# Kernel optimization log

Measured on AMD Instinct MI355X. Metric: run time of the kernel, lower is better.

## Reference

```python
import jax, jax.numpy as jnp
import numpy as np

THRESHOLD = 0.35
NEGPOS_RATIO = 7
VAR0, VAR1 = 0.1, 0.2
NUM_CLASSES = 2


def point_form(pr):
    # center-size [cx,cy,w,h] -> corner [x1,y1,x2,y2]
    return jnp.concatenate([pr[:, :2] - pr[:, 2:] / 2, pr[:, :2] + pr[:, 2:] / 2], axis=1)


def jaccard(a, b):
    # a: [A,4] corner boxes, b: [P,4] corner boxes -> IoU [A,P]
    lt = jnp.maximum(a[:, None, :2], b[None, :, :2])
    rb = jnp.minimum(a[:, None, 2:], b[None, :, 2:])
    wh = jnp.clip(rb - lt, 0.0)
    inter = wh[..., 0] * wh[..., 1]
    area_a = ((a[:, 2] - a[:, 0]) * (a[:, 3] - a[:, 1]))[:, None]
    area_b = ((b[:, 2] - b[:, 0]) * (b[:, 3] - b[:, 1]))[None, :]
    return inter / (area_a + area_b - inter)


def match_one(truths, landms, labels, priors_pf, priors):
    # truths [A,4] corner, landms [A,10], labels [A], priors [P,4] center-size
    A = truths.shape[0]
    overlaps = jaccard(truths, priors_pf)                       # [A,P]
    best_prior_idx = jnp.argmax(overlaps, axis=1)               # [A]
    best_truth_overlap = jnp.max(overlaps, axis=0)              # [P]
    best_truth_idx = jnp.argmax(overlaps, axis=0)               # [P]
    # ensure every gt matches its best prior
    best_truth_overlap = best_truth_overlap.at[best_prior_idx].set(2.0)
    best_truth_idx = best_truth_idx.at[best_prior_idx].set(jnp.arange(A))
    matches = truths[best_truth_idx]                            # [P,4]
    conf = labels[best_truth_idx].astype(jnp.int32)             # [P]
    conf = jnp.where(best_truth_overlap < THRESHOLD, 0, conf)
    # encode loc targets
    g_cxcy = ((matches[:, :2] + matches[:, 2:]) / 2 - priors[:, :2]) / (VAR0 * priors[:, 2:])
    g_wh = jnp.log((matches[:, 2:] - matches[:, :2]) / priors[:, 2:]) / VAR1
    loc = jnp.concatenate([g_cxcy, g_wh], axis=1)               # [P,4]
    # encode landmark targets (5 points)
    ml = landms[best_truth_idx].reshape(-1, 5, 2)               # [P,5,2]
    g_lm = (ml - priors[:, None, :2]) / (VAR0 * priors[:, None, 2:])
    landm = g_lm.reshape(-1, 10)                                # [P,10]
    return loc, conf, landm


def setup_inputs() -> dict:
    key = jax.random.key(0)
    kL, kC, kF, kp1, kp2, kc, ks, klm = jax.random.split(key, 8)
    B, P, A = 32, 131072, 32
    loc_data = jax.random.normal(kL, (B, P, 4), dtype=jnp.float32)
    conf_data = jax.random.normal(kC, (B, P, NUM_CLASSES), dtype=jnp.float32)
    loc_five_data = jax.random.normal(kF, (B, P, 10), dtype=jnp.float32)
    # priors in center-size form with positive w,h
    p_cxy = jax.random.uniform(kp1, (P, 2), minval=0.0, maxval=1.0)
    p_wh = jax.random.uniform(kp2, (P, 2), minval=0.02, maxval=0.3)
    priors = jnp.concatenate([p_cxy, p_wh], axis=1).astype(jnp.float32)
    # targets: [B, A, 15] = 4 corner box coords, 1 label (=1), 10 landmark coords
    g_cxy = jax.random.uniform(kc, (B, A, 2), minval=0.1, maxval=0.9)
    g_wh = jax.random.uniform(ks, (B, A, 2), minval=0.05, maxval=0.4)
    boxes = jnp.concatenate([g_cxy - g_wh / 2, g_cxy + g_wh / 2], axis=-1)
    lbl = jnp.ones((B, A, 1), dtype=jnp.float32)
    lms = jax.random.uniform(klm, (B, A, 10), minval=0.0, maxval=1.0)
    targets = jnp.concatenate([boxes, lbl, lms], axis=-1).astype(jnp.float32)
    return {"loc_data": loc_data, "conf_data": conf_data,
            "loc_five_data": loc_five_data, "priors": priors, "targets": targets}


def multibox_loss(loc_data, conf_data, loc_five_data, priors, targets):
    B, P = loc_data.shape[0], priors.shape[0]
    truths = targets[..., :4]      # [B,A,4]
    labels = targets[..., 4]       # [B,A]
    landms = targets[..., 5:]      # [B,A,10]
    priors_pf = point_form(priors)
    loc_t, conf_t, landm_t = jax.vmap(match_one, in_axes=(0, 0, 0, None, None))(
        truths, landms, labels, priors_pf, priors)   # [B,P,4], [B,P], [B,P,10]

    pos = conf_t > 0               # [B,P]
    posf = pos.astype(loc_data.dtype)

    # localization: smooth L1, sum over positives
    d = loc_data - loc_t
    sl1 = jnp.where(jnp.abs(d) < 1.0, 0.5 * d * d, jnp.abs(d) - 0.5)
    loss_l = jnp.sum(sl1 * posf[..., None])

    # landmarks: MSE, sum over positives
    d5 = loc_five_data - landm_t
    loss_coords = jnp.sum(d5 * d5 * posf[..., None])

    # per-prior classification loss for hard negative mining
    lse = jax.nn.logsumexp(conf_data, axis=-1)                                  # [B,P]
    gt_logit = jnp.take_along_axis(conf_data, conf_t[..., None], axis=-1)[..., 0]
    loss_c_all = lse - gt_logit                                                 # [B,P]
    loss_mine = jnp.where(pos, 0.0, loss_c_all)
    # double-argsort rank trick
    loss_idx = jnp.argsort(-loss_mine, axis=1)
    idx_rank = jnp.argsort(loss_idx, axis=1)
    num_pos = jnp.sum(pos.astype(jnp.int32), axis=1, keepdims=True)             # [B,1]
    num_neg = jnp.minimum(NEGPOS_RATIO * num_pos, P - 1)
    neg = idx_rank < num_neg

    sel = (pos | neg).astype(conf_data.dtype)
    loss_c = jnp.sum(loss_c_all * sel)

    N = jnp.maximum(jnp.sum(num_pos).astype(loc_data.dtype), 1.0)
    return loss_l / N, loss_c / N, loss_coords / N


def reference(loc_data, conf_data, loc_five_data, priors, targets):
    return multibox_loss(loc_data, conf_data, loc_five_data, priors, targets)
```

## Files before the change

### kernel.cpp

```cpp
#include <hip/hip_runtime.h>
#include <stdint.h>
#include <math.h>

#define PP 131072
#define BB 32
#define AA 32
#define THRESH 0.35f

static constexpr size_t OFF_ACCL = 0;
static constexpr size_t OFF_ACCC = 256;
static constexpr size_t OFF_ACCLM = 512;
static constexpr size_t OFF_NP = 768;
static constexpr size_t OFF_SLOT = 1024;
static constexpr size_t OFF_SEL = 9216;
static constexpr size_t OFF_BTI = 16384;
static constexpr size_t OFF_HIST = OFF_BTI;
static constexpr size_t OFF_LM = 16384 + (size_t)BB * PP;

__global__ __launch_bounds__(256) void k_match(
    const float* __restrict__ priors, const float* __restrict__ targets,
    unsigned long long* __restrict__ slots, unsigned char* __restrict__ bti) {
#pragma clang fp contract(off)
  const int b = blockIdx.y;
  const int tid = threadIdx.x;
  __shared__ float tx0[AA], ty0[AA], tx1[AA], ty1[AA], tar[AA];
  if (tid < AA) {
    const float* tg = targets + ((size_t)b * AA + tid) * 15;
    float a0 = tg[0], a1 = tg[1], a2 = tg[2], a3 = tg[3];
    tx0[tid] = a0; ty0[tid] = a1; tx1[tid] = a2; ty1[tid] = a3;
    tar[tid] = (a2 - a0) * (a3 - a1);
  }
  __syncthreads();

  const int base = blockIdx.x * 2048;
  float px0[8], py0[8], px1[8], py1[8], areaB[8];
  float cbi[8], cbd[8];
  int cba[8];
#pragma unroll
  for (int i = 0; i < 8; ++i) {
    const int p = base + i * 256 + tid;
    const float4 pr = reinterpret_cast<const float4*>(priors)[p];
    const float hx = pr.z * 0.5f, hy = pr.w * 0.5f;
    px0[i] = pr.x - hx; py0[i] = pr.y - hy;
    px1[i] = pr.x + hx; py1[i] = pr.y + hy;
    areaB[i] = (px1[i] - px0[i]) * (py1[i] - py0[i]);
    cbi[i] = -1.f; cbd[i] = 1.f; cba[i] = 0;
  }

  const int lane = tid & 63;
  for (int a = 0; a < AA; ++a) {
    const float sx0 = tx0[a], sy0 = ty0[a], sx1 = tx1[a], sy1 = ty1[a];
    const float sar = tar[a];
    float bi = -1.f, bd = 1.f;
    int bp = 0;
#pragma unroll
    for (int i = 0; i < 8; ++i) {
      const float lx = fmaxf(sx0, px0[i]);
      const float ly = fmaxf(sy0, py0[i]);
      const float rx = fminf(sx1, px1[i]);
      const float ry = fminf(sy1, py1[i]);
      const float wx = fmaxf(rx - lx, 0.f);
      const float wy = fmaxf(ry - ly, 0.f);
      const float inter = wx * wy;
      const float den = sar + areaB[i] - inter;
      if (inter * cbd[i] > cbi[i] * den) { cbi[i] = inter; cbd[i] = den; cba[i] = a; }
      if (inter * bd > bi * den) { bi = inter; bd = den; bp = base + i * 256 + tid; }
    }
    const float r = bi / bd;
    unsigned long long key =
        ((unsigned long long)__float_as_uint(r) << 32) |
        (unsigned long long)(0xFFFFFFFFu - (unsigned)bp);
#pragma unroll
    for (int off = 1; off < 64; off <<= 1) {
      unsigned long long o = __shfl_xor(key, off, 64);
      if (o > key) key = o;
    }
    if (lane == 0) atomicMax(&slots[b * AA + a], key);
  }

#pragma unroll
  for (int i = 0; i < 8; ++i) {
    const int p = base + i * 256 + tid;
    const float r = cbi[i] / cbd[i];
    bti[(size_t)b * PP + p] =
        (unsigned char)cba[i] | ((r < THRESH) ? 0 : 32);
  }
}

__global__ __launch_bounds__(256) void k_loss(
    const float* __restrict__ loc, const float* __restrict__ conf,
    const float* __restrict__ loc5, const float* __restrict__ priors,
    const float* __restrict__ targets,
    const unsigned long long* __restrict__ slots,
    const unsigned char* __restrict__ bti, float* __restrict__ lossm,
    double* __restrict__ accL, double* __restrict__ accC,
    double* __restrict__ accLM, int* __restrict__ numpos) {
#pragma clang fp contract(off)
  const int b = blockIdx.y;
  const int tid = threadIdx.x;
  __shared__ float tr[AA][15];
  __shared__ int ovr[AA];
  if (tid < AA) {
    const float* tg = targets + ((size_t)b * AA + tid) * 15;
#pragma unroll
    for (int j = 0; j < 15; ++j) tr[tid][j] = tg[j];
    const unsigned long long key = slots[b * AA + tid];
    ovr[tid] = (int)(0xFFFFFFFFu - (unsigned)(key & 0xFFFFFFFFull));
  }
  __syncthreads();
  int ov[AA];
#pragma unroll
  for (int a = 0; a < AA; ++a) ov[a] = ovr[a];

  double ll = 0.0, lc = 0.0, lm = 0.0;
  int np = 0;
  const int base = blockIdx.x * 2048;
  for (int it = 0; it < 8; ++it) {
    const int p = base + it * 256 + tid;
    const size_t gp = (size_t)b * PP + p;
    const unsigned char f = bti[gp];
    int idx = f & 31;
    bool posf = (f & 32) != 0;
#pragma unroll
    for (int a = 0; a < AA; ++a)
      if (ov[a] == p) { idx = a; posf = true; }
    const int cls = posf ? (int)tr[idx][4] : 0;
    const bool pos = cls > 0;

    const float2 cc = reinterpret_cast<const float2*>(conf)[gp];
    const float mx = fmaxf(cc.x, cc.y);
    const float lse = mx + logf(expf(cc.x - mx) + expf(cc.y - mx));
    const float gtl = (cls >= 1) ? cc.y : cc.x;
    const float lca = lse - gtl;
    lossm[gp] = pos ? 0.f : lca;

    if (pos) {
      ++np;
      lc += (double)lca;
      const float4 pr = reinterpret_cast<const float4*>(priors)[p];
      const float m0 = tr[idx][0], m1 = tr[idx][1];
      const float m2 = tr[idx][2], m3 = tr[idx][3];
      const float vx = 0.1f * pr.z, vy = 0.1f * pr.w;
      const float t0 = ((m0 + m2) / 2.0f - pr.x) / vx;
      const float t1 = ((m1 + m3) / 2.0f - pr.y) / vy;
      const float t2 = logf((m2 - m0) / pr.z) / 0.2f;
      const float t3 = logf((m3 - m1) / pr.w) / 0.2f;
      const float* lp = loc + gp * 4;
      float s = 0.f;
      {
        float d = lp[0] - t0, ad = fabsf(d);
        s += (ad < 1.f) ? 0.5f * d * d : ad - 0.5f;
        d = lp[1] - t1; ad = fabsf(d);
        s += (ad < 1.f) ? 0.5f * d * d : ad - 0.5f;
        d = lp[2] - t2; ad = fabsf(d);
        s += (ad < 1.f) ? 0.5f * d * d : ad - 0.5f;
        d = lp[3] - t3; ad = fabsf(d);
        s += (ad < 1.f) ? 0.5f * d * d : ad - 0.5f;
      }
      ll += (double)s;
      const float* l5 = loc5 + gp * 10;
      float s2 = 0.f;
#pragma unroll
      for (int j = 0; j < 5; ++j) {
        const float tx = (tr[idx][5 + 2 * j] - pr.x) / vx;
        const float ty = (tr[idx][6 + 2 * j] - pr.y) / vy;
        const float dx = l5[2 * j] - tx;
        const float dy = l5[2 * j + 1] - ty;
        s2 += dx * dx + dy * dy;
      }
      lm += (double)s2;
    }
  }
#pragma unroll
  for (int off = 1; off < 64; off <<= 1) {
    ll += __shfl_xor(ll, off, 64);
    lc += __shfl_xor(lc, off, 64);
    lm += __shfl_xor(lm, off, 64);
    np += __shfl_xor(np, off, 64);
  }
  __shared__ double rl[4], rc[4], rm[4];
  __shared__ int rn[4];
  const int wave = tid >> 6, lane = tid & 63;
  if (lane == 0) { rl[wave] = ll; rc[wave] = lc; rm[wave] = lm; rn[wave] = np; }
  __syncthreads();
  if (tid == 0) {
    atomicAdd(&accL[b], rl[0] + rl[1] + rl[2] + rl[3]);
    atomicAdd(&accC[b], rc[0] + rc[1] + rc[2] + rc[3]);
    atomicAdd(&accLM[b], rm[0] + rm[1] + rm[2] + rm[3]);
    atomicAdd(&numpos[b], rn[0] + rn[1] + rn[2] + rn[3]);
  }
}

template <int SHIFT, int BITS>
__global__ __launch_bounds__(256) void k_hist(
    const float* __restrict__ lossm, const unsigned* __restrict__ sel,
    unsigned* __restrict__ hist) {
  const int b = blockIdx.y;
  const int tid = threadIdx.x;
  constexpr int NBINS = 1 << BITS;
  __shared__ unsigned h[NBINS];
  for (int i = tid; i < NBINS; i += 256) h[i] = 0;
  __syncthreads();
  const unsigned hmask =
      (SHIFT + BITS >= 32) ? 0u : (0xFFFFFFFFu << (SHIFT + BITS));
  const unsigned pref = (SHIFT + BITS >= 32) ? 0u : (sel[b * 4] & hmask);
  const float4* v4 = reinterpret_cast<const float4*>(lossm + (size_t)b * PP) +
                     (size_t)blockIdx.x * 4096;
#pragma unroll 4
  for (int k = 0; k < 16; ++k) {
    const float4 x = v4[tid + k * 256];
    const unsigned u0 = __float_as_uint(x.x), u1 = __float_as_uint(x.y);
    const unsigned u2 = __float_as_uint(x.z), u3 = __float_as_uint(x.w);
    if ((u0 & hmask) == pref) atomicAdd(&h[(u0 >> SHIFT) & (NBINS - 1)], 1u);
    if ((u1 & hmask) == pref) atomicAdd(&h[(u1 >> SHIFT) & (NBINS - 1)], 1u);
    if ((u2 & hmask) == pref) atomicAdd(&h[(u2 >> SHIFT) & (NBINS - 1)], 1u);
    if ((u3 & hmask) == pref) atomicAdd(&h[(u3 >> SHIFT) & (NBINS - 1)], 1u);
  }
  __syncthreads();
  unsigned* H = hist + b * 2048;
  for (int i = tid; i < NBINS; i += 256) {
    const unsigned c = h[i];
    if (c) atomicAdd(&H[i], c);
  }
}

template <int SHIFT, int BITS, bool FIRST>
__global__ __launch_bounds__(256) void k_select(
    unsigned* __restrict__ hist, unsigned* __restrict__ sel,
    const int* __restrict__ numpos) {
  const int b = blockIdx.x;
  const int tid = threadIdx.x;
  constexpr int NBINS = 1 << BITS;
  constexpr int CH = NBINS / 256;
  unsigned* H = hist + b * 2048;
  __shared__ unsigned hb[2048];
  __shared__ unsigned csum[256];
  __shared__ unsigned s_krem;
  if (tid == 0) {
    if (FIRST) {
      long long K = 7LL * (long long)numpos[b];
      if (K > PP - 1) K = PP - 1;
      if (K <= 0) {
        s_krem = 0;
        sel[b * 4] = 0xFFFFFFFFu;
        sel[b * 4 + 1] = 0;
      } else {
        s_krem = (unsigned)K;
      }
    } else {
      s_krem = sel[b * 4 + 1];
    }
  }
  for (int i = tid; i < NBINS; i += 256) hb[i] = H[i];
  __syncthreads();
  const int start = NBINS - 1 - tid * CH;
  unsigned msum = 0;
#pragma unroll
  for (int j = 0; j < CH; ++j) msum += hb[start - j];
  csum[tid] = msum;
  for (int i = tid; i < 2048; i += 256) H[i] = 0;
  __syncthreads();
  if (tid == 0) {
    unsigned krem = s_krem;
    if (krem > 0) {
      unsigned cum = 0;
      int c = 0;
      while (c < 255 && cum + csum[c] < krem) { cum += csum[c]; ++c; }
      const int st = NBINS - 1 - c * CH;
      int bin = st - (CH - 1);
      for (int j = 0; j < CH; ++j) {
        const unsigned hh = hb[st - j];
        if (cum + hh >= krem) { bin = st - j; break; }
        cum += hh;
      }
      unsigned pref = FIRST ? 0u : sel[b * 4];
      pref |= ((unsigned)bin) << SHIFT;
      sel[b * 4] = pref;
      sel[b * 4 + 1] = krem - cum;
    }
  }
}

__global__ __launch_bounds__(256) void k_sumtop(
    const float* __restrict__ lossm, const unsigned* __restrict__ sel,
    double* __restrict__ accC) {
  const int b = blockIdx.y;
  const int tid = threadIdx.x;
  const unsigned pref = sel[b * 4];
  const float4* v4 = reinterpret_cast<const float4*>(lossm + (size_t)b * PP) +
                     (size_t)blockIdx.x * 4096;
  double s = 0.0;
#pragma unroll 4
  for (int k = 0; k < 16; ++k) {
    const float4 x = v4[tid + k * 256];
    if (__float_as_uint(x.x) > pref) s += (double)x.x;
    if (__float_as_uint(x.y) > pref) s += (double)x.y;
    if (__float_as_uint(x.z) > pref) s += (double)x.z;
    if (__float_as_uint(x.w) > pref) s += (double)x.w;
  }
#pragma unroll
  for (int off = 1; off < 64; off <<= 1) s += __shfl_xor(s, off, 64);
  __shared__ double rs[4];
  const int wave = tid >> 6, lane = tid & 63;
  if (lane == 0) rs[wave] = s;
  __syncthreads();
  if (tid == 0) atomicAdd(&accC[b], rs[0] + rs[1] + rs[2] + rs[3]);
}

__global__ void k_final(const double* __restrict__ accL,
                        const double* __restrict__ accC,
                        const double* __restrict__ accLM,
                        const int* __restrict__ numpos,
                        const unsigned* __restrict__ sel,
                        float* __restrict__ out) {
  if (threadIdx.x == 0 && blockIdx.x == 0) {
    long long tot = 0;
    double sl = 0, sc = 0, sm = 0;
    for (int b = 0; b < BB; ++b) {
      tot += numpos[b];
      sl += accL[b];
      sc += accC[b];
      const unsigned krem = sel[b * 4 + 1];
      if (krem > 0)
        sc += (double)krem * (double)__uint_as_float(sel[b * 4]);
      sm += accLM[b];
    }
    float N = (float)tot;
    if (N < 1.f) N = 1.f;
    out[0] = (float)(sl / (double)N);
    out[1] = (float)(sc / (double)N);
    out[2] = (float)(sm / (double)N);
  }
}

extern "C" void kernel_launch(void* const* d_in, const int* in_sizes, int n_in,
                              void* d_out, int out_size, void* d_ws,
                              size_t ws_size, hipStream_t stream) {
  const float* loc = (const float*)d_in[0];
  const float* conf = (const float*)d_in[1];
  const float* loc5 = (const float*)d_in[2];
  const float* priors = (const float*)d_in[3];
  const float* tgt = (const float*)d_in[4];
  char* ws = (char*)d_ws;
  double* accL = (double*)(ws + OFF_ACCL);
  double* accC = (double*)(ws + OFF_ACCC);
  double* accLM = (double*)(ws + OFF_ACCLM);
  int* numpos = (int*)(ws + OFF_NP);
  unsigned long long* slots = (unsigned long long*)(ws + OFF_SLOT);
  unsigned char* bti = (unsigned char*)(ws + OFF_BTI);
  float* lossm = (float*)(ws + OFF_LM);
  unsigned* hist = (unsigned*)(ws + OFF_HIST);
  unsigned* sel = (unsigned*)(ws + OFF_SEL);

  hipMemsetAsync(d_ws, 0, OFF_SLOT + (size_t)BB * AA * 8, stream);

  dim3 grid(PP / 2048, BB);
  k_match<<<grid, 256, 0, stream>>>(priors, tgt, slots, bti);
  k_loss<<<grid, 256, 0, stream>>>(loc, conf, loc5, priors, tgt, slots, bti,
                                   lossm, accL, accC, accLM, numpos);
  hipMemsetAsync(ws + OFF_HIST, 0, (size_t)BB * 2048 * 4, stream);
  dim3 hgrid(8, BB);
  k_hist<21, 11><<<hgrid, 256, 0, stream>>>(lossm, sel, hist);
  k_select<21, 11, true><<<BB, 256, 0, stream>>>(hist, sel, numpos);
  k_hist<10, 11><<<hgrid, 256, 0, stream>>>(lossm, sel, hist);
  k_select<10, 11, false><<<BB, 256, 0, stream>>>(hist, sel, numpos);
  k_hist<0, 10><<<hgrid, 256, 0, stream>>>(lossm, sel, hist);
  k_select<0, 10, false><<<BB, 256, 0, stream>>>(hist, sel, numpos);
  k_sumtop<<<hgrid, 256, 0, stream>>>(lossm, sel, accC);
  k_final<<<1, 64, 0, stream>>>(accL, accC, accLM, numpos, sel,
                                (float*)d_out);
}
```

Before: 519.8 us.

## Split per-truth best-prior search into separate kernel and drop atomics

Moves the per-ground-truth best-prior argmax out of the match kernel into its own kernel, where each block scans all priors for two truths and reduces through shared memory with no global 64-bit atomics. A tiny kernel then writes the forced matches into the byte map, so the loss kernel no longer compares every prior against 32 override indices. The cost is a serial 512-block launch that rereads priors, plus an extra launch, while the match kernel loses half its compare work and its atomic traffic.

```diff
diff --git a/kernel.cpp b/kernel.cpp
--- a/kernel.cpp
+++ b/kernel.cpp
@@ -11,15 +11,15 @@
 static constexpr size_t OFF_ACCC = 256;
 static constexpr size_t OFF_ACCLM = 512;
 static constexpr size_t OFF_NP = 768;
-static constexpr size_t OFF_SLOT = 1024;
+static constexpr size_t OFF_OVR = 1024;
 static constexpr size_t OFF_SEL = 9216;
 static constexpr size_t OFF_BTI = 16384;
 static constexpr size_t OFF_HIST = OFF_BTI;
 static constexpr size_t OFF_LM = 16384 + (size_t)BB * PP;
 
-__global__ __launch_bounds__(256) void k_match(
+__global__ __launch_bounds__(256) void k_prior(
     const float* __restrict__ priors, const float* __restrict__ targets,
-    unsigned long long* __restrict__ slots, unsigned char* __restrict__ bti) {
+    unsigned char* __restrict__ bti) {
 #pragma clang fp contract(off)
   const int b = blockIdx.y;
   const int tid = threadIdx.x;
@@ -47,35 +47,17 @@
     cbi[i] = -1.f; cbd[i] = 1.f; cba[i] = 0;
   }
 
-  const int lane = tid & 63;
   for (int a = 0; a < AA; ++a) {
     const float sx0 = tx0[a], sy0 = ty0[a], sx1 = tx1[a], sy1 = ty1[a];
     const float sar = tar[a];
-    float bi = -1.f, bd = 1.f;
-    int bp = 0;
 #pragma unroll
     for (int i = 0; i < 8; ++i) {
-      const float lx = fmaxf(sx0, px0[i]);
-      const float ly = fmaxf(sy0, py0[i]);
-      const float rx = fminf(sx1, px1[i]);
-      const float ry = fminf(sy1, py1[i]);
-      const float wx = fmaxf(rx - lx, 0.f);
-      const float wy = fmaxf(ry - ly, 0.f);
+      const float wx = fmaxf(fminf(sx1, px1[i]) - fmaxf(sx0, px0[i]), 0.f);
+      const float wy = fmaxf(fminf(sy1, py1[i]) - fmaxf(sy0, py0[i]), 0.f);
       const float inter = wx * wy;
       const float den = sar + areaB[i] - inter;
       if (inter * cbd[i] > cbi[i] * den) { cbi[i] = inter; cbd[i] = den; cba[i] = a; }
-      if (inter * bd > bi * den) { bi = inter; bd = den; bp = base + i * 256 + tid; }
-    }
-    const float r = bi / bd;
-    unsigned long long key =
-        ((unsigned long long)__float_as_uint(r) << 32) |
-        (unsigned long long)(0xFFFFFFFFu - (unsigned)bp);
-#pragma unroll
-    for (int off = 1; off < 64; off <<= 1) {
-      unsigned long long o = __shfl_xor(key, off, 64);
-      if (o > key) key = o;
-    }
-    if (lane == 0) atomicMax(&slots[b * AA + a], key);
+    }
   }
 
 #pragma unroll
@@ -87,11 +69,86 @@
   }
 }
 
+__global__ __launch_bounds__(256) void k_truth(
+    const float* __restrict__ priors, const float* __restrict__ targets,
+    unsigned* __restrict__ ovr) {
+#pragma clang fp contract(off)
+  const int b = blockIdx.y;
+  const int a0 = blockIdx.x * 2;
+  const int tid = threadIdx.x;
+  const float* tg0 = targets + ((size_t)b * AA + a0) * 15;
+  const float s0x0 = tg0[0], s0y0 = tg0[1], s0x1 = tg0[2], s0y1 = tg0[3];
+  const float s1x0 = tg0[15], s1y0 = tg0[16], s1x1 = tg0[17], s1y1 = tg0[18];
+  const float sar0 = (s0x1 - s0x0) * (s0y1 - s0y0);
+  const float sar1 = (s1x1 - s1x0) * (s1y1 - s1y0);
+  float bi0 = -1.f, bd0 = 1.f, bi1 = -1.f, bd1 = 1.f;
+  int bp0 = 0, bp1 = 0;
+  const float4* __restrict__ pr4 = reinterpret_cast<const float4*>(priors);
+#pragma unroll 4
+  for (int k = 0; k < PP / 256; ++k) {
+    const int p = k * 256 + tid;
+    const float4 pr = pr4[p];
+    const float hx = pr.z * 0.5f, hy = pr.w * 0.5f;
+    const float px0 = pr.x - hx, py0 = pr.y - hy;
+    const float px1 = pr.x + hx, py1 = pr.y + hy;
+    const float areaB = (px1 - px0) * (py1 - py0);
+    {
+      const float wx = fmaxf(fminf(s0x1, px1) - fmaxf(s0x0, px0), 0.f);
+      const float wy = fmaxf(fminf(s0y1, py1) - fmaxf(s0y0, py0), 0.f);
+      const float inter = wx * wy;
+      const float den = sar0 + areaB - inter;
+      if (inter * bd0 > bi0 * den) { bi0 = inter; bd0 = den; bp0 = p; }
+    }
+    {
+      const float wx = fmaxf(fminf(s1x1, px1) - fmaxf(s1x0, px0), 0.f);
+      const float wy = fmaxf(fminf(s1y1, py1) - fmaxf(s1y0, py0), 0.f);
+      const float inter = wx * wy;
+      const float den = sar1 + areaB - inter;
+      if (inter * bd1 > bi1 * den) { bi1 = inter; bd1 = den; bp1 = p; }
+    }
+  }
+  const float r0 = bi0 / bd0, r1 = bi1 / bd1;
+  unsigned long long k0 =
+      ((unsigned long long)__float_as_uint(r0) << 32) |
+      (unsigned long long)(0xFFFFFFFFu - (unsigned)bp0);
+  unsigned long long k1 =
+      ((unsigned long long)__float_as_uint(r1) << 32) |
+      (unsigned long long)(0xFFFFFFFFu - (unsigned)bp1);
+#pragma unroll
+  for (int off = 1; off < 64; off <<= 1) {
+    unsigned long long o0 = __shfl_xor(k0, off, 64);
+    if (o0 > k0) k0 = o0;
+    unsigned long long o1 = __shfl_xor(k1, off, 64);
+    if (o1 > k1) k1 = o1;
+  }
+  __shared__ unsigned long long red[4][2];
+  const int wv = tid >> 6, lane = tid & 63;
+  if (lane == 0) { red[wv][0] = k0; red[wv][1] = k1; }
+  __syncthreads();
+  if (tid < 2) {
+    unsigned long long m = red[0][tid];
+#pragma unroll
+    for (int w = 1; w < 4; ++w)
+      if (red[w][tid] > m) m = red[w][tid];
+    ovr[b * AA + a0 + tid] = 0xFFFFFFFFu - (unsigned)(m & 0xFFFFFFFFull);
+  }
+}
+
+__global__ void k_override(const unsigned* __restrict__ ovr,
+                           unsigned char* __restrict__ bti) {
+  const int b = threadIdx.x;
+  if (b < BB) {
+    for (int a = 0; a < AA; ++a) {
+      const unsigned p = ovr[b * AA + a];
+      bti[(size_t)b * PP + p] = (unsigned char)(a | 32);
+    }
+  }
+}
+
 __global__ __launch_bounds__(256) void k_loss(
     const float* __restrict__ loc, const float* __restrict__ conf,
     const float* __restrict__ loc5, const float* __restrict__ priors,
     const float* __restrict__ targets,
-    const unsigned long long* __restrict__ slots,
     const unsigned char* __restrict__ bti, float* __restrict__ lossm,
     double* __restrict__ accL, double* __restrict__ accC,
     double* __restrict__ accLM, int* __restrict__ numpos) {
@@ -99,18 +156,12 @@
   const int b = blockIdx.y;
   const int tid = threadIdx.x;
   __shared__ float tr[AA][15];
-  __shared__ int ovr[AA];
   if (tid < AA) {
     const float* tg = targets + ((size_t)b * AA + tid) * 15;
 #pragma unroll
     for (int j = 0; j < 15; ++j) tr[tid][j] = tg[j];
-    const unsigned long long key = slots[b * AA + tid];
-    ovr[tid] = (int)(0xFFFFFFFFu - (unsigned)(key & 0xFFFFFFFFull));
-  }
-  __syncthreads();
-  int ov[AA];
-#pragma unroll
-  for (int a = 0; a < AA; ++a) ov[a] = ovr[a];
+  }
+  __syncthreads();
 
   double ll = 0.0, lc = 0.0, lm = 0.0;
   int np = 0;
@@ -119,11 +170,8 @@
     const int p = base + it * 256 + tid;
     const size_t gp = (size_t)b * PP + p;
     const unsigned char f = bti[gp];
-    int idx = f & 31;
-    bool posf = (f & 32) != 0;
-#pragma unroll
-    for (int a = 0; a < AA; ++a)
-      if (ov[a] == p) { idx = a; posf = true; }
+    const int idx = f & 31;
+    const bool posf = (f & 32) != 0;
     const int cls = posf ? (int)tr[idx][4] : 0;
     const bool pos = cls > 0;
 
@@ -346,17 +394,19 @@
   double* accC = (double*)(ws + OFF_ACCC);
   double* accLM = (double*)(ws + OFF_ACCLM);
   int* numpos = (int*)(ws + OFF_NP);
-  unsigned long long* slots = (unsigned long long*)(ws + OFF_SLOT);
+  unsigned* ovr = (unsigned*)(ws + OFF_OVR);
   unsigned char* bti = (unsigned char*)(ws + OFF_BTI);
   float* lossm = (float*)(ws + OFF_LM);
   unsigned* hist = (unsigned*)(ws + OFF_HIST);
   unsigned* sel = (unsigned*)(ws + OFF_SEL);
 
-  hipMemsetAsync(d_ws, 0, OFF_SLOT + (size_t)BB * AA * 8, stream);
+  hipMemsetAsync(d_ws, 0, 1024, stream);
 
   dim3 grid(PP / 2048, BB);
-  k_match<<<grid, 256, 0, stream>>>(priors, tgt, slots, bti);
-  k_loss<<<grid, 256, 0, stream>>>(loc, conf, loc5, priors, tgt, slots, bti,
+  k_prior<<<grid, 256, 0, stream>>>(priors, tgt, bti);
+  k_truth<<<dim3(AA / 2, BB), 256, 0, stream>>>(priors, tgt, ovr);
+  k_override<<<1, 64, 0, stream>>>(ovr, bti);
+  k_loss<<<grid, 256, 0, stream>>>(loc, conf, loc5, priors, tgt, bti,
                                    lossm, accL, accC, accLM, numpos);
   hipMemsetAsync(ws + OFF_HIST, 0, (size_t)BB * 2048 * 4, stream);
   dim3 hgrid(8, BB);
```

New measurement: 522.1 us. About the same (+0.4%).

## Fuse radix-select histogram passes into loss kernel and drop global atomics in matching

Applied to the files above, without the earlier changes.

The first radix histogram is now built in shared memory inside the loss kernel. Each select scan is folded into the next histogram or sum kernel, which removes separate select launches and one full pass over the loss buffer. Per-truth best-prior search now reduces within the block through shared memory and writes per-block partials instead of using 64-bit global atomicMax. A small kernel then writes the forced matches directly into the byte map, so the loss kernel no longer compares each prior against 32 overrides. The cost is redundant scanning of the histogram by every block and extra shared-memory atomics in the loss kernel.

```diff
diff --git a/kernel.cpp b/kernel.cpp
--- a/kernel.cpp
+++ b/kernel.cpp
@@ -11,19 +11,27 @@
 static constexpr size_t OFF_ACCC = 256;
 static constexpr size_t OFF_ACCLM = 512;
 static constexpr size_t OFF_NP = 768;
-static constexpr size_t OFF_SLOT = 1024;
-static constexpr size_t OFF_SEL = 9216;
-static constexpr size_t OFF_BTI = 16384;
-static constexpr size_t OFF_HIST = OFF_BTI;
-static constexpr size_t OFF_LM = 16384 + (size_t)BB * PP;
-
-__global__ __launch_bounds__(256) void k_match(
+static constexpr size_t OFF_SEL1 = 1024;
+static constexpr size_t OFF_SEL2 = 1280;
+static constexpr size_t OFF_SEL3 = 1536;
+static constexpr size_t OFF_GPART = 4096;
+static constexpr size_t OFF_H1 = (size_t)1 << 20;
+static constexpr size_t OFF_H2 = OFF_H1 + (size_t)BB * 2048 * 4;
+static constexpr size_t OFF_H3 = OFF_H2 + (size_t)BB * 2048 * 4;
+static constexpr size_t OFF_BTI = (size_t)2 << 20;
+static constexpr size_t OFF_LM = (size_t)8 << 20;
+
+__global__ __launch_bounds__(256) void k_match2(
     const float* __restrict__ priors, const float* __restrict__ targets,
-    unsigned long long* __restrict__ slots, unsigned char* __restrict__ bti) {
+    unsigned char* __restrict__ bti, unsigned long long* __restrict__ gpart) {
 #pragma clang fp contract(off)
   const int b = blockIdx.y;
   const int tid = threadIdx.x;
   __shared__ float tx0[AA], ty0[AA], tx1[AA], ty1[AA], tar[AA];
+  __shared__ float rbi[AA][65], rbd[AA][65];
+  __shared__ int rbp[AA][65];
+  __shared__ float r2bi[AA][9], r2bd[AA][9];
+  __shared__ int r2bp[AA][9];
   if (tid < AA) {
     const float* tg = targets + ((size_t)b * AA + tid) * 15;
     float a0 = tg[0], a1 = tg[1], a2 = tg[2], a3 = tg[3];
@@ -47,7 +55,6 @@
     cbi[i] = -1.f; cbd[i] = 1.f; cba[i] = 0;
   }
 
-  const int lane = tid & 63;
   for (int a = 0; a < AA; ++a) {
     const float sx0 = tx0[a], sy0 = ty0[a], sx1 = tx1[a], sy1 = ty1[a];
     const float sar = tar[a];
@@ -55,35 +62,95 @@
     int bp = 0;
 #pragma unroll
     for (int i = 0; i < 8; ++i) {
-      const float lx = fmaxf(sx0, px0[i]);
-      const float ly = fmaxf(sy0, py0[i]);
-      const float rx = fminf(sx1, px1[i]);
-      const float ry = fminf(sy1, py1[i]);
-      const float wx = fmaxf(rx - lx, 0.f);
-      const float wy = fmaxf(ry - ly, 0.f);
+      const float wx = fmaxf(fminf(sx1, px1[i]) - fmaxf(sx0, px0[i]), 0.f);
+      const float wy = fmaxf(fminf(sy1, py1[i]) - fmaxf(sy0, py0[i]), 0.f);
       const float inter = wx * wy;
       const float den = sar + areaB[i] - inter;
       if (inter * cbd[i] > cbi[i] * den) { cbi[i] = inter; cbd[i] = den; cba[i] = a; }
       if (inter * bd > bi * den) { bi = inter; bd = den; bp = base + i * 256 + tid; }
     }
-    const float r = bi / bd;
-    unsigned long long key =
-        ((unsigned long long)__float_as_uint(r) << 32) |
-        (unsigned long long)(0xFFFFFFFFu - (unsigned)bp);
-#pragma unroll
-    for (int off = 1; off < 64; off <<= 1) {
-      unsigned long long o = __shfl_xor(key, off, 64);
-      if (o > key) key = o;
-    }
-    if (lane == 0) atomicMax(&slots[b * AA + a], key);
+#pragma unroll
+    for (int off = 1; off <= 2; off <<= 1) {
+      const float obi = __shfl_xor(bi, off, 64);
+      const float obd = __shfl_xor(bd, off, 64);
+      const int obp = __shfl_xor(bp, off, 64);
+      const float l = obi * bd, r = bi * obd;
+      const bool take = (l > r) || (l == r && obp < bp);
+      bi = take ? obi : bi; bd = take ? obd : bd; bp = take ? obp : bp;
+    }
+    if ((tid & 3) == 0) {
+      rbi[a][tid >> 2] = bi; rbd[a][tid >> 2] = bd; rbp[a][tid >> 2] = bp;
+    }
   }
 
 #pragma unroll
   for (int i = 0; i < 8; ++i) {
     const int p = base + i * 256 + tid;
     const float r = cbi[i] / cbd[i];
-    bti[(size_t)b * PP + p] =
-        (unsigned char)cba[i] | ((r < THRESH) ? 0 : 32);
+    bti[(size_t)b * PP + p] = (unsigned char)cba[i] | ((r < THRESH) ? 0 : 32);
+  }
+
+  __syncthreads();
+  {
+    const int a = tid & 31, c = tid >> 5;
+    float bi = rbi[a][c * 8], bd = rbd[a][c * 8];
+    int bp = rbp[a][c * 8];
+#pragma unroll
+    for (int j = 1; j < 8; ++j) {
+      const float obi = rbi[a][c * 8 + j], obd = rbd[a][c * 8 + j];
+      const int obp = rbp[a][c * 8 + j];
+      const float l = obi * bd, r = bi * obd;
+      const bool take = (l > r) || (l == r && obp < bp);
+      bi = take ? obi : bi; bd = take ? obd : bd; bp = take ? obp : bp;
+    }
+    r2bi[a][c] = bi; r2bd[a][c] = bd; r2bp[a][c] = bp;
+  }
+  __syncthreads();
+  if (tid < AA) {
+    float bi = r2bi[tid][0], bd = r2bd[tid][0];
+    int bp = r2bp[tid][0];
+#pragma unroll
+    for (int j = 1; j < 8; ++j) {
+      const float obi = r2bi[tid][j], obd = r2bd[tid][j];
+      const int obp = r2bp[tid][j];
+      const float l = obi * bd, r = bi * obd;
+      const bool take = (l > r) || (l == r && obp < bp);
+      bi = take ? obi : bi; bd = take ? obd : bd; bp = take ? obp : bp;
+    }
+    const float r = bi / bd;
+    const unsigned long long key =
+        ((unsigned long long)__float_as_uint(r) << 32) |
+        (unsigned long long)(0xFFFFFFFFu - (unsigned)bp);
+    gpart[((size_t)b * AA + tid) * 64 + blockIdx.x] = key;
+  }
+}
+
+__global__ __launch_bounds__(256) void k_truthapply(
+    const unsigned long long* __restrict__ gpart,
+    unsigned char* __restrict__ bti) {
+  const int b = blockIdx.x;
+  const int tid = threadIdx.x;
+  __shared__ unsigned long long p2[AA][9];
+  __shared__ unsigned ovp[AA];
+  {
+    const int a = tid >> 3, j = tid & 7;
+    const unsigned long long* g = gpart + ((size_t)b * AA + a) * 64 + j * 8;
+    unsigned long long m = g[0];
+#pragma unroll
+    for (int k = 1; k < 8; ++k) if (g[k] > m) m = g[k];
+    p2[a][j] = m;
+  }
+  __syncthreads();
+  if (tid < AA) {
+    unsigned long long m = p2[tid][0];
+#pragma unroll
+    for (int k = 1; k < 8; ++k) if (p2[tid][k] > m) m = p2[tid][k];
+    ovp[tid] = 0xFFFFFFFFu - (unsigned)(m & 0xFFFFFFFFull);
+  }
+  __syncthreads();
+  if (tid == 0) {
+    for (int a = 0; a < AA; ++a)
+      bti[(size_t)b * PP + ovp[a]] = (unsigned char)(a | 32);
   }
 }
 
@@ -91,26 +158,22 @@
     const float* __restrict__ loc, const float* __restrict__ conf,
     const float* __restrict__ loc5, const float* __restrict__ priors,
     const float* __restrict__ targets,
-    const unsigned long long* __restrict__ slots,
     const unsigned char* __restrict__ bti, float* __restrict__ lossm,
+    unsigned* __restrict__ H1,
     double* __restrict__ accL, double* __restrict__ accC,
     double* __restrict__ accLM, int* __restrict__ numpos) {
 #pragma clang fp contract(off)
   const int b = blockIdx.y;
   const int tid = threadIdx.x;
   __shared__ float tr[AA][15];
-  __shared__ int ovr[AA];
+  __shared__ unsigned h[2048];
+  for (int i = tid; i < 2048; i += 256) h[i] = 0;
   if (tid < AA) {
     const float* tg = targets + ((size_t)b * AA + tid) * 15;
 #pragma unroll
     for (int j = 0; j < 15; ++j) tr[tid][j] = tg[j];
-    const unsigned long long key = slots[b * AA + tid];
-    ovr[tid] = (int)(0xFFFFFFFFu - (unsigned)(key & 0xFFFFFFFFull));
-  }
-  __syncthreads();
-  int ov[AA];
-#pragma unroll
-  for (int a = 0; a < AA; ++a) ov[a] = ovr[a];
+  }
+  __syncthreads();
 
   double ll = 0.0, lc = 0.0, lm = 0.0;
   int np = 0;
@@ -119,11 +182,8 @@
     const int p = base + it * 256 + tid;
     const size_t gp = (size_t)b * PP + p;
     const unsigned char f = bti[gp];
-    int idx = f & 31;
-    bool posf = (f & 32) != 0;
-#pragma unroll
-    for (int a = 0; a < AA; ++a)
-      if (ov[a] == p) { idx = a; posf = true; }
+    const int idx = f & 31;
+    const bool posf = (f & 32) != 0;
     const int cls = posf ? (int)tr[idx][4] : 0;
     const bool pos = cls > 0;
 
@@ -132,7 +192,9 @@
     const float lse = mx + logf(expf(cc.x - mx) + expf(cc.y - mx));
     const float gtl = (cls >= 1) ? cc.y : cc.x;
     const float lca = lse - gtl;
-    lossm[gp] = pos ? 0.f : lca;
+    const float v = pos ? 0.f : lca;
+    lossm[gp] = v;
+    atomicAdd(&h[__float_as_uint(v) >> 21], 1u);
 
     if (pos) {
       ++np;
@@ -189,21 +251,59 @@
     atomicAdd(&accLM[b], rm[0] + rm[1] + rm[2] + rm[3]);
     atomicAdd(&numpos[b], rn[0] + rn[1] + rn[2] + rn[3]);
   }
-}
-
-template <int SHIFT, int BITS>
-__global__ __launch_bounds__(256) void k_hist(
-    const float* __restrict__ lossm, const unsigned* __restrict__ sel,
-    unsigned* __restrict__ hist) {
+  unsigned* Hb = H1 + b * 2048;
+  for (int i = tid; i < 2048; i += 256) {
+    const unsigned c = h[i];
+    if (c) atomicAdd(&Hb[i], c);
+  }
+}
+
+template <int NBINS>
+__device__ __forceinline__ void selscan(const unsigned* __restrict__ H,
+                                        unsigned krem_in, unsigned* s_out,
+                                        unsigned* hb, unsigned* csum,
+                                        int tid) {
+  constexpr int CH = NBINS / 256;
+  for (int i = tid; i < NBINS; i += 256) hb[i] = H[i];
+  __syncthreads();
+  const int start = NBINS - 1 - tid * CH;
+  unsigned msum = 0;
+#pragma unroll
+  for (int j = 0; j < CH; ++j) msum += hb[start - j];
+  csum[tid] = msum;
+  __syncthreads();
+  if (tid == 0) {
+    unsigned cum = 0;
+    int c = 0;
+    while (c < 255 && cum + csum[c] < krem_in) { cum += csum[c]; ++c; }
+    const int st = NBINS - 1 - c * CH;
+    int bin = st - (CH - 1);
+    for (int j = 0; j < CH; ++j) {
+      const unsigned hh = hb[st - j];
+      if (cum + hh >= krem_in) { bin = st - j; break; }
+      cum += hh;
+    }
+    s_out[0] = (unsigned)bin;
+    s_out[1] = krem_in - cum;
+  }
+  __syncthreads();
+}
+
+__global__ __launch_bounds__(256) void k_hist2sel(
+    const float* __restrict__ lossm, const unsigned* __restrict__ H1,
+    unsigned* __restrict__ H2, const int* __restrict__ numpos,
+    unsigned* __restrict__ sel1) {
   const int b = blockIdx.y;
   const int tid = threadIdx.x;
-  constexpr int NBINS = 1 << BITS;
-  __shared__ unsigned h[NBINS];
-  for (int i = tid; i < NBINS; i += 256) h[i] = 0;
-  __syncthreads();
-  const unsigned hmask =
-      (SHIFT + BITS >= 32) ? 0u : (0xFFFFFFFFu << (SHIFT + BITS));
-  const unsigned pref = (SHIFT + BITS >= 32) ? 0u : (sel[b * 4] & hmask);
+  __shared__ unsigned hb[2048], csum[256], sout[2], h[2048];
+  long long K = 7LL * (long long)numpos[b];
+  if (K > PP - 1) K = PP - 1;
+  if (K < 0) K = 0;
+  selscan<2048>(H1 + b * 2048, (unsigned)K, sout, hb, csum, tid);
+  const unsigned bin1 = sout[0], krem1 = sout[1];
+  if (blockIdx.x == 0 && tid == 0) { sel1[b * 2] = bin1; sel1[b * 2 + 1] = krem1; }
+  for (int i = tid; i < 2048; i += 256) h[i] = 0;
+  __syncthreads();
   const float4* v4 = reinterpret_cast<const float4*>(lossm + (size_t)b * PP) +
                      (size_t)blockIdx.x * 4096;
 #pragma unroll 4
@@ -211,82 +311,69 @@
     const float4 x = v4[tid + k * 256];
     const unsigned u0 = __float_as_uint(x.x), u1 = __float_as_uint(x.y);
     const unsigned u2 = __float_as_uint(x.z), u3 = __float_as_uint(x.w);
-    if ((u0 & hmask) == pref) atomicAdd(&h[(u0 >> SHIFT) & (NBINS - 1)], 1u);
-    if ((u1 & hmask) == pref) atomicAdd(&h[(u1 >> SHIFT) & (NBINS - 1)], 1u);
-    if ((u2 & hmask) == pref) atomicAdd(&h[(u2 >> SHIFT) & (NBINS - 1)], 1u);
-    if ((u3 & hmask) == pref) atomicAdd(&h[(u3 >> SHIFT) & (NBINS - 1)], 1u);
-  }
-  __syncthreads();
-  unsigned* H = hist + b * 2048;
-  for (int i = tid; i < NBINS; i += 256) {
+    if ((u0 >> 21) == bin1) atomicAdd(&h[(u0 >> 10) & 2047], 1u);
+    if ((u1 >> 21) == bin1) atomicAdd(&h[(u1 >> 10) & 2047], 1u);
+    if ((u2 >> 21) == bin1) atomicAdd(&h[(u2 >> 10) & 2047], 1u);
+    if ((u3 >> 21) == bin1) atomicAdd(&h[(u3 >> 10) & 2047], 1u);
+  }
+  __syncthreads();
+  unsigned* Hb = H2 + b * 2048;
+  for (int i = tid; i < 2048; i += 256) {
     const unsigned c = h[i];
-    if (c) atomicAdd(&H[i], c);
-  }
-}
-
-template <int SHIFT, int BITS, bool FIRST>
-__global__ __launch_bounds__(256) void k_select(
-    unsigned* __restrict__ hist, unsigned* __restrict__ sel,
-    const int* __restrict__ numpos) {
-  const int b = blockIdx.x;
-  const int tid = threadIdx.x;
-  constexpr int NBINS = 1 << BITS;
-  constexpr int CH = NBINS / 256;
-  unsigned* H = hist + b * 2048;
-  __shared__ unsigned hb[2048];
-  __shared__ unsigned csum[256];
-  __shared__ unsigned s_krem;
-  if (tid == 0) {
-    if (FIRST) {
-      long long K = 7LL * (long long)numpos[b];
-      if (K > PP - 1) K = PP - 1;
-      if (K <= 0) {
-        s_krem = 0;
-        sel[b * 4] = 0xFFFFFFFFu;
-        sel[b * 4 + 1] = 0;
-      } else {
-        s_krem = (unsigned)K;
-      }
-    } else {
-      s_krem = sel[b * 4 + 1];
-    }
-  }
-  for (int i = tid; i < NBINS; i += 256) hb[i] = H[i];
-  __syncthreads();
-  const int start = NBINS - 1 - tid * CH;
-  unsigned msum = 0;
-#pragma unroll
-  for (int j = 0; j < CH; ++j) msum += hb[start - j];
-  csum[tid] = msum;
-  for (int i = tid; i < 2048; i += 256) H[i] = 0;
-  __syncthreads();
-  if (tid == 0) {
-    unsigned krem = s_krem;
-    if (krem > 0) {
-      unsigned cum = 0;
-      int c = 0;
-      while (c < 255 && cum + csum[c] < krem) { cum += csum[c]; ++c; }
-      const int st = NBINS - 1 - c * CH;
-      int bin = st - (CH - 1);
-      for (int j = 0; j < CH; ++j) {
-        const unsigned hh = hb[st - j];
-        if (cum + hh >= krem) { bin = st - j; break; }
-        cum += hh;
-      }
-      unsigned pref = FIRST ? 0u : sel[b * 4];
-      pref |= ((unsigned)bin) << SHIFT;
-      sel[b * 4] = pref;
-      sel[b * 4 + 1] = krem - cum;
-    }
-  }
-}
-
-__global__ __launch_bounds__(256) void k_sumtop(
-    const float* __restrict__ lossm, const unsigned* __restrict__ sel,
-    double* __restrict__ accC) {
+    if (c) atomicAdd(&Hb[i], c);
+  }
+}
+
+__global__ __launch_bounds__(256) void k_hist3sel(
+    const float* __restrict__ lossm, const unsigned* __restrict__ H2,
+    unsigned* __restrict__ H3, const unsigned* __restrict__ sel1,
+    unsigned* __restrict__ sel2) {
   const int b = blockIdx.y;
   const int tid = threadIdx.x;
-  const unsigned pref = sel[b * 4];
+  __shared__ unsigned hb[2048], csum[256], sout[2], h[1024];
+  const unsigned bin1 = sel1[b * 2], krem1 = sel1[b * 2 + 1];
+  selscan<2048>(H2 + b * 2048, krem1, sout, hb, csum, tid);
+  const unsigned bin2 = sout[0], krem2 = sout[1];
+  if (blockIdx.x == 0 && tid == 0) { sel2[b * 2] = bin2; sel2[b * 2 + 1] = krem2; }
+  for (int i = tid; i < 1024; i += 256) h[i] = 0;
+  __syncthreads();
+  const float4* v4 = reinterpret_cast<const float4*>(lossm + (size_t)b * PP) +
+                     (size_t)blockIdx.x * 4096;
+#pragma unroll 4
+  for (int k = 0; k < 16; ++k) {
+    const float4 x = v4[tid + k * 256];
+    const unsigned u0 = __float_as_uint(x.x), u1 = __float_as_uint(x.y);
+    const unsigned u2 = __float_as_uint(x.z), u3 = __float_as_uint(x.w);
+    if ((u0 >> 21) == bin1 && ((u0 >> 10) & 2047) == bin2)
+      atomicAdd(&h[u0 & 1023], 1u);
+    if ((u1 >> 21) == bin1 && ((u1 >> 10) & 2047) == bin2)
+      atomicAdd(&h[u1 & 1023], 1u);
+    if ((u2 >> 21) == bin1 && ((u2 >> 10) & 2047) == bin2)
+      atomicAdd(&h[u2 & 1023], 1u);
+    if ((u3 >> 21) == bin1 && ((u3 >> 10) & 2047) == bin2)
+      atomicAdd(&h[u3 & 1023], 1u);
+  }
+  __syncthreads();
+  unsigned* Hb = H3 + b * 2048;
+  for (int i = tid; i < 1024; i += 256) {
+    const unsigned c = h[i];
+    if (c) atomicAdd(&Hb[i], c);
+  }
+}
+
+__global__ __launch_bounds__(256) void k_sumtop2(
+    const float* __restrict__ lossm, const unsigned* __restrict__ H3,
+    const unsigned* __restrict__ sel1, const unsigned* __restrict__ sel2,
+    unsigned* __restrict__ sel3, double* __restrict__ accC) {
+  const int b = blockIdx.y;
+  const int tid = threadIdx.x;
+  __shared__ unsigned hb[1024], csum[256], sout[2];
+  const unsigned bin1 = sel1[b * 2];
+  const unsigned bin2 = sel2[b * 2], krem2 = sel2[b * 2 + 1];
+  selscan<1024>(H3 + b * 2048, krem2, sout, hb, csum, tid);
+  const unsigned bin3 = sout[0], krem3 = sout[1];
+  const unsigned pref = (bin1 << 21) | (bin2 << 10) | bin3;
+  if (blockIdx.x == 0 && tid == 0) { sel3[b * 2] = pref; sel3[b * 2 + 1] = krem3; }
   const float4* v4 = reinterpret_cast<const float4*>(lossm + (size_t)b * PP) +
                      (size_t)blockIdx.x * 4096;
   double s = 0.0;
@@ -311,7 +398,7 @@
                         const double* __restrict__ accC,
                         const double* __restrict__ accLM,
                         const int* __restrict__ numpos,
-                        const unsigned* __restrict__ sel,
+                        const unsigned* __restrict__ sel3,
                         float* __restrict__ out) {
   if (threadIdx.x == 0 && blockIdx.x == 0) {
     long long tot = 0;
@@ -320,9 +407,9 @@
       tot += numpos[b];
       sl += accL[b];
       sc += accC[b];
-      const unsigned krem = sel[b * 4 + 1];
+      const unsigned krem = sel3[b * 2 + 1];
       if (krem > 0)
-        sc += (double)krem * (double)__uint_as_float(sel[b * 4]);
+        sc += (double)krem * (double)__uint_as_float(sel3[b * 2]);
       sm += accLM[b];
     }
     float N = (float)tot;
@@ -346,27 +433,28 @@
   double* accC = (double*)(ws + OFF_ACCC);
   double* accLM = (double*)(ws + OFF_ACCLM);
   int* numpos = (int*)(ws + OFF_NP);
-  unsigned long long* slots = (unsigned long long*)(ws + OFF_SLOT);
+  unsigned* sel1 = (unsigned*)(ws + OFF_SEL1);
+  unsigned* sel2 = (unsigned*)(ws + OFF_SEL2);
+  unsigned* sel3 = (unsigned*)(ws + OFF_SEL3);
+  unsigned long long* gpart = (unsigned long long*)(ws + OFF_GPART);
+  unsigned* H1 = (unsigned*)(ws + OFF_H1);
+  unsigned* H2 = (unsigned*)(ws + OFF_H2);
+  unsigned* H3 = (unsigned*)(ws + OFF_H3);
   unsigned char* bti = (unsigned char*)(ws + OFF_BTI);
   float* lossm = (float*)(ws + OFF_LM);
-  unsigned* hist = (unsigned*)(ws + OFF_HIST);
-  unsigned* sel = (unsigned*)(ws + OFF_SEL);
-
-  hipMemsetAsync(d_ws, 0, OFF_SLOT + (size_t)BB * AA * 8, stream);
+
+  hipMemsetAsync(ws, 0, 2048, stream);
+  hipMemsetAsync(ws + OFF_H1, 0, (size_t)3 * BB * 2048 * 4, stream);
 
   dim3 grid(PP / 2048, BB);
-  k_match<<<grid, 256, 0, stream>>>(priors, tgt, slots, bti);
-  k_loss<<<grid, 256, 0, stream>>>(loc, conf, loc5, priors, tgt, slots, bti,
-                                   lossm, accL, accC, accLM, numpos);
-  hipMemsetAsync(ws + OFF_HIST, 0, (size_t)BB * 2048 * 4, stream);
+  k_match2<<<grid, 256, 0, stream>>>(priors, tgt, bti, gpart);
+  k_truthapply<<<BB, 256, 0, stream>>>(gpart, bti);
+  k_loss<<<grid, 256, 0, stream>>>(loc, conf, loc5, priors, tgt, bti, lossm,
+                                   H1, accL, accC, accLM, numpos);
   dim3 hgrid(8, BB);
-  k_hist<21, 11><<<hgrid, 256, 0, stream>>>(lossm, sel, hist);
-  k_select<21, 11, true><<<BB, 256, 0, stream>>>(hist, sel, numpos);
-  k_hist<10, 11><<<hgrid, 256, 0, stream>>>(lossm, sel, hist);
-  k_select<10, 11, false><<<BB, 256, 0, stream>>>(hist, sel, numpos);
-  k_hist<0, 10><<<hgrid, 256, 0, stream>>>(lossm, sel, hist);
-  k_select<0, 10, false><<<BB, 256, 0, stream>>>(hist, sel, numpos);
-  k_sumtop<<<hgrid, 256, 0, stream>>>(lossm, sel, accC);
-  k_final<<<1, 64, 0, stream>>>(accL, accC, accLM, numpos, sel,
+  k_hist2sel<<<hgrid, 256, 0, stream>>>(lossm, H1, H2, numpos, sel1);
+  k_hist3sel<<<hgrid, 256, 0, stream>>>(lossm, H2, H3, sel1, sel2);
+  k_sumtop2<<<hgrid, 256, 0, stream>>>(lossm, H3, sel1, sel2, sel3, accC);
+  k_final<<<1, 64, 0, stream>>>(accL, accC, accLM, numpos, sel3,
                                 (float*)d_out);
 }
```

Result: faster. 445.7 us (-14.3%).
